# Kernel optimization log

Hardware: AMD Instinct MI355X
Metric: run time of the kernel (lower is better)

Reference implementation:

```python
import jax, jax.numpy as jnp
import numpy as np

NUM_HEADS = 16
REF_CLUSTER = 0
TOP_RATIO = 0.3        # adaptive_sparsity(layer_idx=0) = min_sparsity
FRAME_SUBSAMPLE = 0.7  # frame_subsample_ratio in the torch code


def setup_inputs() -> dict:
    key = jax.random.key(0)
    k0, k1, k2 = jax.random.split(key, 3)
    B, S, P, C = 1, 32, 512, 1024
    N = S * P
    K, Fc = 4, 8  # K clusters of Fc frames each
    x = jax.random.normal(k0, (B, N, C), dtype=jnp.float32)
    W_qkv = jax.random.normal(k1, (C, 3 * C), dtype=jnp.float32) * (C ** -0.5)
    b_qkv = jnp.zeros((3 * C,), jnp.float32)
    W_proj = jax.random.normal(k2, (C, C), dtype=jnp.float32) * (C ** -0.5)
    b_proj = jnp.zeros((C,), jnp.float32)
    clusters = jnp.arange(S, dtype=jnp.int32).reshape(K, Fc)  # disjoint frame clusters
    keyframes = clusters[:, 0]  # one keyframe per cluster
    return {"x": x, "W_qkv": W_qkv, "b_qkv": b_qkv, "W_proj": W_proj,
            "b_proj": b_proj, "clusters": clusters, "keyframes": keyframes}


def _attn(q, k, v, scale):
    # flash_attn_func math: softmax(q k^T / sqrt(D)) v
    logits = jnp.einsum('bhqd,bhkd->bhqk', q, k) * scale
    return jnp.einsum('bhqk,bhkd->bhqd', jax.nn.softmax(logits, axis=-1), v)


def reference(x, W_qkv, b_qkv, W_proj, b_proj, clusters, keyframes):
    B, N, C = x.shape
    H = NUM_HEADS
    D = C // H
    K, Fc = clusters.shape
    S = K * Fc
    P = N // S
    scale = D ** -0.5

    # qkv projection -> q,k,v each [B, H, S, P, D]
    qkv = (x @ W_qkv + b_qkv).reshape(B, N, 3, H, D)
    q, k, v = [jnp.transpose(qkv[:, :, i], (0, 2, 1, 3)).reshape(B, H, S, P, D)
               for i in range(3)]

    # coarse: keyframe prototype scores -> topk patches per cluster
    q_proto = q[:, :, keyframes]  # [B,H,K,P,D]
    k_proto = k[:, :, keyframes]
    attn_score = jnp.mean(jnp.max(jnp.sum(k_proto * q_proto, axis=-1), axis=1), axis=0)  # [K,P]
    tk = max(1, int(P * TOP_RATIO))
    _, patch_idx = jax.lax.top_k(attn_score, tk)  # [K, tk]

    n_sub = max(1, int(Fc * FRAME_SUBSAMPLE))
    out_frames = jnp.zeros((B, H, S, P, D), x.dtype)
    for ci in range(K):
        frame_ids = clusters[ci]
        q_local = q[:, :, frame_ids].reshape(B, H, Fc * P, D)
        k_parts, v_parts = [], []
        for nc in range(K):
            # deterministic stand-in for torch.randperm frame subsampling
            sampled = clusters[nc] if nc in (REF_CLUSTER, ci) else clusters[nc][:n_sub]
            pidx = patch_idx[nc]
            k_parts.append(k[:, :, sampled][:, :, :, pidx].reshape(B, H, -1, D))
            v_parts.append(v[:, :, sampled][:, :, :, pidx].reshape(B, H, -1, D))
        k_local = jnp.concatenate(k_parts, axis=2)
        v_local = jnp.concatenate(v_parts, axis=2)
        out_local = _attn(q_local, k_local, v_local, scale).reshape(B, H, Fc, P, D)
        out_frames = out_frames.at[:, :, frame_ids].add(out_local)

    out = jnp.transpose(out_frames.reshape(B, H, N, D), (0, 2, 1, 3)).reshape(B, N, C)
    return out @ W_proj + b_proj
```

## Files before the change

kernel.cpp:

```cpp
#include <hip/hip_runtime.h>
#include <hip/hip_bf16.h>
#include <hip/hip_fp16.h>

#define DEVINL __device__ __forceinline__

using short8 = __attribute__((ext_vector_type(8))) short;
using half8  = __attribute__((ext_vector_type(8))) _Float16;
using half2v = __attribute__((ext_vector_type(2))) _Float16;
using f32x4  = __attribute__((ext_vector_type(4))) float;
using uint4v = __attribute__((ext_vector_type(4))) unsigned;

static constexpr int N_TOK = 16384;
static constexpr int NH    = 16;
static constexpr int HD    = 64;
static constexpr int KCL   = 4;
static constexpr int TK    = 153;
static constexpr int LMAX  = 4096;

typedef __attribute__((address_space(1))) unsigned GU32;
typedef __attribute__((address_space(3))) unsigned LU32;

DEVINL void gload16(const void* g, void* l) {
    __builtin_amdgcn_global_load_lds((const GU32*)g, (LU32*)l, 16, 0, 0);
}

#if __has_builtin(__builtin_amdgcn_exp2f)
#define EXP2(x) __builtin_amdgcn_exp2f(x)
#else
#define EXP2(x) exp2f(x)
#endif

DEVINL void plswap32(unsigned& a, unsigned& b) {
#if __has_builtin(__builtin_amdgcn_permlane32_swap)
    auto r = __builtin_amdgcn_permlane32_swap(a, b, false, false);
    a = r[0]; b = r[1];
#else
    asm volatile("v_permlane32_swap_b32 %0, %1" : "+v"(a), "+v"(b));
#endif
}
DEVINL void plswap16(unsigned& a, unsigned& b) {
#if __has_builtin(__builtin_amdgcn_permlane16_swap)
    auto r = __builtin_amdgcn_permlane16_swap(a, b, false, false);
    a = r[0]; b = r[1];
#else
    asm volatile("v_permlane16_swap_b32 %0, %1" : "+v"(a), "+v"(b));
#endif
}

DEVINL unsigned short f2bf(float f) {
    unsigned u = __float_as_uint(f);
    unsigned r = u + 0x7FFFu + ((u >> 16) & 1u);
    return (unsigned short)(r >> 16);
}
DEVINL float bf2f(unsigned short h) { return __uint_as_float(((unsigned)h) << 16); }

__global__ void prep_w_kernel(const float* __restrict__ W, short* __restrict__ Btp,
                              int ncols) {
    int total = ncols * 2048;
    for (int o = blockIdx.x * blockDim.x + threadIdx.x; o < total;
         o += gridDim.x * blockDim.x) {
        int j = o >> 11, k = o & 2047, kk = k & 1023;
        float w = W[(size_t)kk * ncols + j];
        unsigned short hv = f2bf(w);
        unsigned short r = (k < 1024) ? hv : f2bf(w - bf2f(hv));
        Btp[o] = (short)r;
    }
}

template <int EPI>
__global__ __launch_bounds__(256)
void gemm_split(const float* __restrict__ xf32, const _Float16* __restrict__ xf16,
                const short* __restrict__ Btp, const float* __restrict__ bias,
                int nbn, _Float16* __restrict__ qkvh, float* __restrict__ protoF,
                float* __restrict__ outF) {
    __shared__ short Ah[4096], Al[4096], Bh[4096], Bl[4096];
    int tid = threadIdx.x, wid = tid >> 6;
    int lane = tid & 63, lr = lane & 15, lg = lane >> 4;
    int bid = blockIdx.x;
    int nb = bid % nbn, mb = bid / nbn;
    int m0 = mb * 128, n0 = nb * 128;
    int wm = wid >> 1, wn = wid & 1;

    f32x4 acc[4][4];
#pragma unroll
    for (int i = 0; i < 4; i++)
#pragma unroll
        for (int j = 0; j < 4; j++)
#pragma unroll
            for (int r = 0; r < 4; r++) acc[i][j][r] = 0.f;

    int arow = tid >> 1, ahalf = (tid & 1) * 16;
    int brow = tid >> 2, bcc = tid & 3;

    for (int kk0 = 0; kk0 < 1024; kk0 += 32) {
        gload16(Btp + (size_t)(n0 + brow) * 2048 + kk0 + bcc * 8, Bh + wid * 512);
        gload16(Btp + (size_t)(n0 + 64 + brow) * 2048 + kk0 + bcc * 8, Bh + 2048 + wid * 512);
        gload16(Btp + (size_t)(n0 + brow) * 2048 + 1024 + kk0 + bcc * 8, Bl + wid * 512);
        gload16(Btp + (size_t)(n0 + 64 + brow) * 2048 + 1024 + kk0 + bcc * 8, Bl + 2048 + wid * 512);

        float fv[16];
        if constexpr (EPI == 0) {
            const float* src = xf32 + (size_t)(m0 + arow) * 1024 + kk0 + ahalf;
#pragma unroll
            for (int q = 0; q < 4; q++) {
                f32x4 t = *(const f32x4*)(src + q * 4);
#pragma unroll
                for (int j = 0; j < 4; j++) fv[q * 4 + j] = t[j];
            }
        } else {
            const _Float16* src = xf16 + (size_t)(kk0 >> 6) * ((size_t)N_TOK * HD)
                                  + (size_t)(m0 + arow) * 64 + (kk0 & 63) + ahalf;
            half8 g0 = *(const half8*)(src), g1 = *(const half8*)(src + 8);
#pragma unroll
            for (int j = 0; j < 8; j++) { fv[j] = (float)g0[j]; fv[8 + j] = (float)g1[j]; }
        }
        short8 h8[2], l8[2];
#pragma unroll
        for (int q = 0; q < 2; q++)
#pragma unroll
            for (int j = 0; j < 8; j++) {
                float v = fv[q * 8 + j];
                unsigned short hv = f2bf(v);
                h8[q][j] = (short)hv;
                l8[q][j] = (short)f2bf(v - bf2f(hv));
            }
        *(short8*)(Ah + arow * 32 + ahalf)     = h8[0];
        *(short8*)(Ah + arow * 32 + ahalf + 8) = h8[1];
        *(short8*)(Al + arow * 32 + ahalf)     = l8[0];
        *(short8*)(Al + arow * 32 + ahalf + 8) = l8[1];
        __syncthreads();

        short8 ah[4], al[4], bh[4], bl[4];
#pragma unroll
        for (int mi = 0; mi < 4; mi++) {
            int ro = (wm * 64 + mi * 16 + lr) * 32 + lg * 8;
            ah[mi] = *(const short8*)(Ah + ro);
            al[mi] = *(const short8*)(Al + ro);
        }
#pragma unroll
        for (int ni = 0; ni < 4; ni++) {
            int ro = (wn * 64 + ni * 16 + lr) * 32 + lg * 8;
            bh[ni] = *(const short8*)(Bh + ro);
            bl[ni] = *(const short8*)(Bl + ro);
        }
#pragma unroll
        for (int mi = 0; mi < 4; mi++)
#pragma unroll
            for (int ni = 0; ni < 4; ni++) {
                acc[mi][ni] = __builtin_amdgcn_mfma_f32_16x16x32_bf16(ah[mi], bh[ni], acc[mi][ni], 0, 0, 0);
                acc[mi][ni] = __builtin_amdgcn_mfma_f32_16x16x32_bf16(al[mi], bh[ni], acc[mi][ni], 0, 0, 0);
                acc[mi][ni] = __builtin_amdgcn_mfma_f32_16x16x32_bf16(ah[mi], bl[ni], acc[mi][ni], 0, 0, 0);
            }
        __syncthreads();
    }

#pragma unroll
    for (int mi = 0; mi < 4; mi++) {
#pragma unroll
        for (int ni = 0; ni < 4; ni++) {
            int col = n0 + wn * 64 + ni * 16 + lr;
            float bv = bias[col];
#pragma unroll
            for (int r = 0; r < 4; r++) {
                int rowm = m0 + wm * 64 + mi * 16 + lg * 4 + r;
                float val = acc[mi][ni][r] + bv;
                if constexpr (EPI == 0) {
                    int i3 = col >> 10, h = (col >> 6) & 15, d = col & 63;
                    qkvh[(((size_t)i3 * NH + h) * N_TOK + rowm) * HD + d] = (_Float16)val;
                    int s = rowm >> 9;
                    if (i3 < 2 && (s & 7) == 0) {
                        int kf = s >> 3, p = rowm & 511;
                        protoF[(((size_t)i3 * KCL + kf) * 512 + p) * (NH * HD) + h * HD + d] = val;
                    }
                } else {
                    outF[(size_t)rowm * 1024 + col] = val;
                }
            }
        }
    }
}

__global__ __launch_bounds__(256)
void score_kernel(const float* __restrict__ protoF, float* __restrict__ scores) {
    int tid = threadIdx.x, lane = tid & 63;
    int pos = blockIdx.x * 4 + (tid >> 6);
    int kc = pos >> 9, p = pos & 511;
    const float* qp = protoF + ((size_t)kc * 512 + p) * (NH * HD);
    const float* kp = protoF + ((size_t)(KCL + kc) * 512 + p) * (NH * HD);
    int hh = lane >> 2, dp = (lane & 3) * 16;
    float sum = 0.f;
#pragma unroll
    for (int i = 0; i < 16; i++) sum += qp[hh * 64 + dp + i] * kp[hh * 64 + dp + i];
    sum += __shfl_xor(sum, 1, 64);
    sum += __shfl_xor(sum, 2, 64);
    float v = ((lane & 3) == 0) ? sum : -1e30f;
    for (int m = 4; m < 64; m <<= 1) v = fmaxf(v, __shfl_xor(v, m, 64));
    if (lane == 0) scores[pos] = v;
}

__global__ __launch_bounds__(64)
void topk_kernel(const float* __restrict__ scores, int* __restrict__ pidx) {
    int ci = blockIdx.x, lane = threadIdx.x;
    float v[8];
#pragma unroll
    for (int m = 0; m < 8; m++) v[m] = scores[ci * 512 + lane * 8 + m];
    for (int i = 0; i < TK; i++) {
        float best = -1e30f; int bj = 0;
#pragma unroll
        for (int m = 0; m < 8; m++) if (v[m] > best) { best = v[m]; bj = m; }
        int bidx = lane * 8 + bj;
        for (int mk = 1; mk < 64; mk <<= 1) {
            float ov = __shfl_xor(best, mk, 64);
            int   oi = __shfl_xor(bidx, mk, 64);
            if (ov > best || (ov == best && oi < bidx)) { best = ov; bidx = oi; }
        }
        bool own = ((bidx >> 3) == lane);
        int sel = bidx - lane * 8;
#pragma unroll
        for (int m = 0; m < 8; m++) if (own && m == sel) v[m] = -1e30f;
        if (lane == 0) pidx[ci * TK + i] = bidx;
    }
}

__global__ __launch_bounds__(256)
void nlist_kernel(const int* __restrict__ pidx, int* __restrict__ nlist) {
    int ci = blockIdx.x;
    int L = TK * (ci == 0 ? 23 : 26);
    for (int pos = threadIdx.x; pos < L; pos += 256) {
        int seg = pos / TK, j = pos - seg * TK;
        int nc = 0, fi = 0, acc = 0;
        for (int c = 0; c < 4; c++) {
            int cnt = (c == 0 || c == ci) ? 8 : 5;
            if (seg >= acc && seg < acc + cnt) { nc = c; fi = seg - acc; }
            acc += cnt;
        }
        nlist[ci * LMAX + pos] = (nc * 8 + fi) * 512 + pidx[nc * TK + j];
    }
}

__global__ __launch_bounds__(256)
void gatherv_kernel(const _Float16* __restrict__ qkvh, const int* __restrict__ nlist,
                    _Float16* __restrict__ vT) {
    __shared__ _Float16 vrow[64 * 80];
    int bid = blockIdx.x;
    int t64 = bid & 63, h = (bid >> 6) & 15, ci = bid >> 10;
    int L = TK * (ci == 0 ? 23 : 26);
    const _Float16* vsrc = qkvh + (size_t)2 * NH * N_TOK * HD + (size_t)h * N_TOK * HD;
    int tid = threadIdx.x;
#pragma unroll
    for (int rep = 0; rep < 2; rep++) {
        int c = rep * 256 + tid; int row = c >> 3, cc = c & 7;
        int kvg = t64 * 64 + row;
        half8 val;
#pragma unroll
        for (int j = 0; j < 8; j++) val[j] = (_Float16)0.f;
        if (kvg < L) {
            int n = nlist[ci * LMAX + kvg];
            val = *(const half8*)(vsrc + (size_t)n * HD + cc * 8);
        }
        *(half8*)(vrow + row * 80 + cc * 8) = val;
    }
    __syncthreads();
#pragma unroll
    for (int rep = 0; rep < 2; rep++) {
        int c = rep * 256 + tid; int d = c >> 3, kvc = c & 7;
        half8 ov;
#pragma unroll
        for (int j = 0; j < 8; j++) ov[j] = vrow[(kvc * 8 + j) * 80 + d];
        *(half8*)(vT + ((size_t)(ci * 16 + h) * 64 + d) * LMAX + t64 * 64 + kvc * 8) = ov;
    }
}

__global__ __launch_bounds__(512)
void attn_kernel(const _Float16* __restrict__ qkvh, const _Float16* __restrict__ vT,
                 const int* __restrict__ nlist, _Float16* __restrict__ outh) {
    __shared__ _Float16 kt[2][4096];
    __shared__ _Float16 vt[2][4096];
    int bid = blockIdx.x;
    int qb = bid & 15, h = (bid >> 4) & 15, ci = bid >> 8;
    int tid = threadIdx.x, wid = tid >> 6, lane = tid & 63;
    int lr = lane & 15, lg = lane >> 4;
    int L = TK * (ci == 0 ? 23 : 26);
    int nt = (L + 63) >> 6;

    const _Float16* qh = qkvh;
    const _Float16* kh = qkvh + (size_t)NH * N_TOK * HD;
    int qrow0 = ci * 4096 + qb * 256 + wid * 32;

    const _Float16 qsc = (_Float16)0.180336880f;
    half8 qf[2][2];
#pragma unroll
    for (int g = 0; g < 2; g++)
#pragma unroll
        for (int ks = 0; ks < 2; ks++) {
            qf[g][ks] = *(const half8*)(qh + ((size_t)h * N_TOK + qrow0 + g * 16 + lr) * HD
                                        + ks * 32 + lg * 8);
#pragma unroll
            for (int j = 0; j < 8; j++) qf[g][ks][j] *= qsc;
        }
    half8 ones;
#pragma unroll
    for (int j = 0; j < 8; j++) ones[j] = (_Float16)1.f;

    f32x4 o[2][4], lacc[2];
    float mrun[2];
#pragma unroll
    for (int g = 0; g < 2; g++) {
#pragma unroll
        for (int nd = 0; nd < 4; nd++)
#pragma unroll
            for (int r = 0; r < 4; r++) o[g][nd][r] = 0.f;
#pragma unroll
        for (int r = 0; r < 4; r++) lacc[g][r] = 0.f;
        mrun[g] = -1e30f;
    }

    int krow = tid >> 3, kcc = tid & 7;
    int swz = (kcc ^ (krow & 7)) * 8;
    const int* nl = nlist + ci * LMAX;
    const _Float16* vTb = vT + ((size_t)(ci * 16 + h) * 64 + krow) * LMAX;
    size_t khbase = (size_t)h * N_TOK;

    int n_cur = (krow < L) ? nl[krow] : 0;
    gload16(kh + (khbase + n_cur) * HD + swz, &kt[0][wid * 512]);
    gload16(vTb + swz, &vt[0][wid * 512]);
    int kvg1 = 64 + krow;
    int n_nxt = (kvg1 < L) ? nl[kvg1] : 0;

    for (int t = 0; t < nt; t++) {
        asm volatile("s_waitcnt vmcnt(0)" ::: "memory");
        __builtin_amdgcn_sched_barrier(0);
        __builtin_amdgcn_s_barrier();
        __builtin_amdgcn_sched_barrier(0);

        if (t + 1 < nt) {
            gload16(kh + (khbase + n_nxt) * HD + swz, &kt[(t + 1) & 1][wid * 512]);
            gload16(vTb + (t + 1) * 64 + swz, &vt[(t + 1) & 1][wid * 512]);
            int kvg2 = (t + 2) * 64 + krow;
            n_nxt = (kvg2 < L) ? nl[kvg2] : 0;
        }

        const _Float16* ktb = kt[t & 1];
        const _Float16* vtb = vt[t & 1];

        f32x4 s[2][4];
#pragma unroll
        for (int g = 0; g < 2; g++)
#pragma unroll
            for (int ni = 0; ni < 4; ni++)
#pragma unroll
                for (int r = 0; r < 4; r++) s[g][ni][r] = 0.f;
#pragma unroll
        for (int ni = 0; ni < 4; ni++)
#pragma unroll
            for (int ks = 0; ks < 2; ks++) {
                int row = ni * 16 + lr;
                half8 kb = *(const half8*)(ktb + row * 64 + (((ks * 4 + lg) ^ (row & 7)) * 8));
                s[0][ni] = __builtin_amdgcn_mfma_f32_16x16x32_f16(kb, qf[0][ks], s[0][ni], 0, 0, 0);
                s[1][ni] = __builtin_amdgcn_mfma_f32_16x16x32_f16(kb, qf[1][ks], s[1][ni], 0, 0, 0);
            }
        if (t == nt - 1) {
#pragma unroll
            for (int ni = 0; ni < 4; ni++) {
                int kvv = t * 64 + ni * 16 + lg * 4;
#pragma unroll
                for (int r = 0; r < 4; r++)
                    if (kvv + r >= L) { s[0][ni][r] = -1e30f; s[1][ni][r] = -1e30f; }
            }
        }

        float mloc[2];
#pragma unroll
        for (int g = 0; g < 2; g++) {
            float m0 = fmaxf(fmaxf(s[g][0][0], s[g][0][1]), fmaxf(s[g][0][2], s[g][0][3]));
            float m1 = fmaxf(fmaxf(s[g][1][0], s[g][1][1]), fmaxf(s[g][1][2], s[g][1][3]));
            float m2 = fmaxf(fmaxf(s[g][2][0], s[g][2][1]), fmaxf(s[g][2][2], s[g][2][3]));
            float m3 = fmaxf(fmaxf(s[g][3][0], s[g][3][1]), fmaxf(s[g][3][2], s[g][3][3]));
            mloc[g] = fmaxf(fmaxf(m0, m1), fmaxf(m2, m3));
        }
        bool ok = (mloc[0] <= mrun[0] + 8.f) && (mloc[1] <= mrun[1] + 8.f);
        if (!__all(ok)) {
#pragma unroll
            for (int g = 0; g < 2; g++) {
                float mt = mloc[g];
                mt = fmaxf(mt, __shfl_xor(mt, 16, 64));
                mt = fmaxf(mt, __shfl_xor(mt, 32, 64));
                float mn = fmaxf(mrun[g], mt);
                float corr = EXP2(mrun[g] - mn);
                mrun[g] = mn;
#pragma unroll
                for (int r = 0; r < 4; r++) lacc[g][r] *= corr;
#pragma unroll
                for (int nd = 0; nd < 4; nd++)
#pragma unroll
                    for (int r = 0; r < 4; r++) o[g][nd][r] *= corr;
            }
        }

        half8 pf[2][2];
#pragma unroll
        for (int g = 0; g < 2; g++) {
            float p[4][4];
#pragma unroll
            for (int ni = 0; ni < 4; ni++)
#pragma unroll
                for (int r = 0; r < 4; r++) p[ni][r] = EXP2(s[g][ni][r] - mrun[g]);
            unsigned c[4][2];
#pragma unroll
            for (int ni = 0; ni < 4; ni++) {
                c[ni][0] = __builtin_bit_cast(unsigned, __builtin_amdgcn_cvt_pkrtz(p[ni][0], p[ni][1]));
                c[ni][1] = __builtin_bit_cast(unsigned, __builtin_amdgcn_cvt_pkrtz(p[ni][2], p[ni][3]));
            }
#pragma unroll
            for (int ksv = 0; ksv < 2; ksv++) {
                unsigned a0 = c[2 * ksv][0], a1 = c[2 * ksv][1];
                unsigned b0 = c[2 * ksv + 1][0], b1 = c[2 * ksv + 1][1];
                plswap32(a0, b0); plswap32(a1, b1);
                plswap16(a0, b0); plswap16(a1, b1);
                uint4v w = {a0, a1, b0, b1};
                pf[g][ksv] = __builtin_bit_cast(half8, w);
            }
        }

#pragma unroll
        for (int nd = 0; nd < 4; nd++)
#pragma unroll
            for (int ksv = 0; ksv < 2; ksv++) {
                int row = nd * 16 + lr;
                half8 vb = *(const half8*)(vtb + row * 64 + (((ksv * 4 + lg) ^ (row & 7)) * 8));
                o[0][nd] = __builtin_amdgcn_mfma_f32_16x16x32_f16(vb, pf[0][ksv], o[0][nd], 0, 0, 0);
                o[1][nd] = __builtin_amdgcn_mfma_f32_16x16x32_f16(vb, pf[1][ksv], o[1][nd], 0, 0, 0);
            }
#pragma unroll
        for (int g = 0; g < 2; g++)
#pragma unroll
            for (int ksv = 0; ksv < 2; ksv++)
                lacc[g] = __builtin_amdgcn_mfma_f32_16x16x32_f16(ones, pf[g][ksv], lacc[g], 0, 0, 0);
    }

#pragma unroll
    for (int g = 0; g < 2; g++) {
        float inv = 1.f / lacc[g][0];
        int qg = qrow0 + g * 16 + lr;
        unsigned* dst = (unsigned*)(outh + (size_t)h * N_TOK * HD + (size_t)qg * 64);
#pragma unroll
        for (int nd = 0; nd < 4; nd++)
#pragma unroll
            for (int rp = 0; rp < 2; rp++) {
                half2v hv;
                hv[0] = (_Float16)(o[g][nd][2 * rp] * inv);
                hv[1] = (_Float16)(o[g][nd][2 * rp + 1] * inv);
                dst[(nd * 16 + lg * 4) / 2 + rp] = __builtin_bit_cast(unsigned, hv);
            }
    }
}

extern "C" void kernel_launch(void* const* d_in, const int* in_sizes, int n_in,
                              void* d_out, int out_size, void* d_ws, size_t ws_size,
                              hipStream_t stream) {
    (void)in_sizes; (void)n_in; (void)out_size;
    const float* x     = (const float*)d_in[0];
    const float* Wqkv  = (const float*)d_in[1];
    const float* bqkv  = (const float*)d_in[2];
    const float* Wproj = (const float*)d_in[3];
    const float* bproj = (const float*)d_in[4];

    char* ws = (char*)d_ws;
    size_t off = 0;
    auto alloc = [&](size_t bytes) -> void* {
        void* p = ws + off; off += (bytes + 255) & ~(size_t)255; return p;
    };
    short*    Btp1   = (short*)alloc((size_t)3072 * 2048 * 2);
    short*    Btp2   = (short*)alloc((size_t)1024 * 2048 * 2);
    _Float16* qkvh   = (_Float16*)alloc((size_t)3 * NH * N_TOK * HD * 2);
    void*     R1     = alloc((size_t)KCL * NH * HD * LMAX * 2);
    float*    scores = (float*)alloc((size_t)KCL * 512 * 4);
    int*      pidx   = (int*)alloc((size_t)KCL * TK * 4);
    int*      nlist  = (int*)alloc((size_t)KCL * LMAX * 4);
    if (ws_size < off) return;

    float*    protoF = (float*)R1;
    _Float16* vT     = (_Float16*)R1;
    _Float16* vout   = qkvh + (size_t)2 * NH * N_TOK * HD;

    prep_w_kernel<<<2048, 256, 0, stream>>>(Wqkv, Btp1, 3072);
    prep_w_kernel<<<1024, 256, 0, stream>>>(Wproj, Btp2, 1024);

    gemm_split<0><<<128 * 24, 256, 0, stream>>>(x, nullptr, Btp1, bqkv, 24,
                                                qkvh, protoF, nullptr);

    score_kernel<<<512, 256, 0, stream>>>(protoF, scores);
    topk_kernel<<<4, 64, 0, stream>>>(scores, pidx);
    nlist_kernel<<<4, 256, 0, stream>>>(pidx, nlist);
    gatherv_kernel<<<4096, 256, 0, stream>>>(qkvh, nlist, vT);

    attn_kernel<<<1024, 512, 0, stream>>>(qkvh, vT, nlist, vout);

    gemm_split<1><<<128 * 8, 256, 0, stream>>>(nullptr, vout, Btp2, bproj, 8,
                                               nullptr, nullptr, (float*)d_out);
}
```

Before: 1.085 ms.

## Double-buffer split-bf16 GEMM tiles to overlap global loads with MFMA

Shared-memory tiles for A and B (high and low bf16 parts) are now double-buffered. The next K-step's B async loads and A register loads are issued before the current step's MFMAs, and the converted A tile is written to the other buffer afterwards. This drops one barrier per iteration and hides global-load latency behind compute. The cost is doubled LDS use (64KB per block), which may lower occupancy, plus extra registers to hold the prefetched A values. The A thread mapping is also changed to coalesce loads as row-quarter chunks.

```diff
diff --git a/kernel.cpp b/kernel.cpp
--- a/kernel.cpp
+++ b/kernel.cpp
@@ -73,7 +73,7 @@
                 const short* __restrict__ Btp, const float* __restrict__ bias,
                 int nbn, _Float16* __restrict__ qkvh, float* __restrict__ protoF,
                 float* __restrict__ outF) {
-    __shared__ short Ah[4096], Al[4096], Bh[4096], Bl[4096];
+    __shared__ short Ah[2][4096], Al[2][4096], Bh[2][4096], Bl[2][4096];
     int tid = threadIdx.x, wid = tid >> 6;
     int lane = tid & 63, lr = lane & 15, lg = lane >> 4;
     int bid = blockIdx.x;
@@ -89,59 +89,79 @@
 #pragma unroll
             for (int r = 0; r < 4; r++) acc[i][j][r] = 0.f;
 
-    int arow = tid >> 1, ahalf = (tid & 1) * 16;
     int brow = tid >> 2, bcc = tid & 3;
-
-    for (int kk0 = 0; kk0 < 1024; kk0 += 32) {
-        gload16(Btp + (size_t)(n0 + brow) * 2048 + kk0 + bcc * 8, Bh + wid * 512);
-        gload16(Btp + (size_t)(n0 + 64 + brow) * 2048 + kk0 + bcc * 8, Bh + 2048 + wid * 512);
-        gload16(Btp + (size_t)(n0 + brow) * 2048 + 1024 + kk0 + bcc * 8, Bl + wid * 512);
-        gload16(Btp + (size_t)(n0 + 64 + brow) * 2048 + 1024 + kk0 + bcc * 8, Bl + 2048 + wid * 512);
-
-        float fv[16];
-        if constexpr (EPI == 0) {
-            const float* src = xf32 + (size_t)(m0 + arow) * 1024 + kk0 + ahalf;
-#pragma unroll
-            for (int q = 0; q < 4; q++) {
-                f32x4 t = *(const f32x4*)(src + q * 4);
-#pragma unroll
-                for (int j = 0; j < 4; j++) fv[q * 4 + j] = t[j];
-            }
-        } else {
-            const _Float16* src = xf16 + (size_t)(kk0 >> 6) * ((size_t)N_TOK * HD)
-                                  + (size_t)(m0 + arow) * 64 + (kk0 & 63) + ahalf;
-            half8 g0 = *(const half8*)(src), g1 = *(const half8*)(src + 8);
-#pragma unroll
-            for (int j = 0; j < 8; j++) { fv[j] = (float)g0[j]; fv[8 + j] = (float)g1[j]; }
-        }
-        short8 h8[2], l8[2];
-#pragma unroll
-        for (int q = 0; q < 2; q++)
+    int arow = tid >> 2, acol = tid & 3;
+
+    float fva[2][8];
+
+    auto issueB = [&](int kt, int buf) {
+        int kk0 = kt * 32;
+        gload16(Btp + (size_t)(n0 + brow) * 2048 + kk0 + bcc * 8, &Bh[buf][wid * 512]);
+        gload16(Btp + (size_t)(n0 + 64 + brow) * 2048 + kk0 + bcc * 8, &Bh[buf][2048 + wid * 512]);
+        gload16(Btp + (size_t)(n0 + brow) * 2048 + 1024 + kk0 + bcc * 8, &Bl[buf][wid * 512]);
+        gload16(Btp + (size_t)(n0 + 64 + brow) * 2048 + 1024 + kk0 + bcc * 8, &Bl[buf][2048 + wid * 512]);
+    };
+    auto loadA = [&](int kt) {
+        int kk0 = kt * 32;
+#pragma unroll
+        for (int p = 0; p < 2; p++) {
+            int row = m0 + p * 64 + arow;
+            int k = kk0 + acol * 8;
+            if constexpr (EPI == 0) {
+                const float* src = xf32 + (size_t)row * 1024 + k;
+                f32x4 t0 = *(const f32x4*)src;
+                f32x4 t1 = *(const f32x4*)(src + 4);
+#pragma unroll
+                for (int j = 0; j < 4; j++) { fva[p][j] = t0[j]; fva[p][4 + j] = t1[j]; }
+            } else {
+                const _Float16* src = xf16 + (size_t)(k >> 6) * ((size_t)N_TOK * HD)
+                                      + (size_t)row * 64 + (k & 63);
+                half8 g = *(const half8*)src;
+#pragma unroll
+                for (int j = 0; j < 8; j++) fva[p][j] = (float)g[j];
+            }
+        }
+    };
+    auto writeA = [&](int buf) {
+#pragma unroll
+        for (int p = 0; p < 2; p++) {
+            short8 h8, l8;
 #pragma unroll
             for (int j = 0; j < 8; j++) {
-                float v = fv[q * 8 + j];
+                float v = fva[p][j];
                 unsigned short hv = f2bf(v);
-                h8[q][j] = (short)hv;
-                l8[q][j] = (short)f2bf(v - bf2f(hv));
-            }
-        *(short8*)(Ah + arow * 32 + ahalf)     = h8[0];
-        *(short8*)(Ah + arow * 32 + ahalf + 8) = h8[1];
-        *(short8*)(Al + arow * 32 + ahalf)     = l8[0];
-        *(short8*)(Al + arow * 32 + ahalf + 8) = l8[1];
-        __syncthreads();
+                h8[j] = (short)hv;
+                l8[j] = (short)f2bf(v - bf2f(hv));
+            }
+            *(short8*)(&Ah[buf][p * 2048 + tid * 8]) = h8;
+            *(short8*)(&Al[buf][p * 2048 + tid * 8]) = l8;
+        }
+    };
+
+    issueB(0, 0);
+    loadA(0);
+    writeA(0);
+    __syncthreads();
+
+    for (int kt = 0; kt < 32; ++kt) {
+        int cur = kt & 1, nxt = cur ^ 1;
+        if (kt + 1 < 32) {
+            issueB(kt + 1, nxt);
+            loadA(kt + 1);
+        }
 
         short8 ah[4], al[4], bh[4], bl[4];
 #pragma unroll
         for (int mi = 0; mi < 4; mi++) {
             int ro = (wm * 64 + mi * 16 + lr) * 32 + lg * 8;
-            ah[mi] = *(const short8*)(Ah + ro);
-            al[mi] = *(const short8*)(Al + ro);
+            ah[mi] = *(const short8*)(&Ah[cur][ro]);
+            al[mi] = *(const short8*)(&Al[cur][ro]);
         }
 #pragma unroll
         for (int ni = 0; ni < 4; ni++) {
             int ro = (wn * 64 + ni * 16 + lr) * 32 + lg * 8;
-            bh[ni] = *(const short8*)(Bh + ro);
-            bl[ni] = *(const short8*)(Bl + ro);
+            bh[ni] = *(const short8*)(&Bh[cur][ro]);
+            bl[ni] = *(const short8*)(&Bl[cur][ro]);
         }
 #pragma unroll
         for (int mi = 0; mi < 4; mi++)
@@ -151,6 +171,8 @@
                 acc[mi][ni] = __builtin_amdgcn_mfma_f32_16x16x32_bf16(al[mi], bh[ni], acc[mi][ni], 0, 0, 0);
                 acc[mi][ni] = __builtin_amdgcn_mfma_f32_16x16x32_bf16(ah[mi], bl[ni], acc[mi][ni], 0, 0, 0);
             }
+
+        if (kt + 1 < 32) writeA(nxt);
         __syncthreads();
     }
 
```

Result: slower. 1.114 ms (+2.7%).
